# Kernel tuning notes

Measured on AMD Instinct MI355X. Metric: run time of the kernel, lower is better.

## Reference

```python
import jax, jax.numpy as jnp
import numpy as np

N, E, K = 20000, 320000, 4
IN, HID, OUT, HD = 512, 256, 128, 256


def setup_inputs() -> dict:
    key = jax.random.key(0)
    ks = jax.random.split(key, 12)
    def lin(k, fi, fo):
        return jax.random.normal(k, (fi, fo), jnp.float32) / np.sqrt(fi)
    return {
        "x": jax.random.normal(ks[0], (N, IN), jnp.float32),
        "edge_index": jax.random.randint(ks[1], (K, 2, E), 0, N),
        "value": jax.random.normal(ks[2], (K, 3), jnp.float32),
        "index": jax.random.randint(ks[3], (K, 2), 0, N),
        "W1": lin(ks[4], IN, HID),  "b1": jnp.zeros((HID,), jnp.float32),
        "W2": lin(ks[5], HID, OUT), "b2": jnp.zeros((OUT,), jnp.float32),
        "Wd": lin(ks[6], 2 * OUT + 3, HD), "bd": jnp.zeros((HD,), jnp.float32),
        "Wp": lin(ks[7], HD, 1),    "bp": jnp.zeros((1,), jnp.float32),
    }


def reference(x, edge_index, value, index, W1, b1, W2, b2, Wd, bd, Wp, bp):
    n = x.shape[0]
    loops = jnp.arange(n)

    def gcn(h, src, dst, W, b):
        # GCNConv: symmetric normalization with self-loops already in src/dst
        deg = jnp.zeros((n,), h.dtype).at[dst].add(1.0)
        dinv = jnp.where(deg > 0, deg ** -0.5, 0.0)
        norm = dinv[src] * dinv[dst]                      # [E+N]
        msg = (h @ W)[src] * norm[:, None]                # [E+N, F_out]
        return jnp.zeros((n, W.shape[1]), h.dtype).at[dst].add(msg) + b

    def encode(ei):
        src = jnp.concatenate([ei[0], loops])             # add self-loops
        dst = jnp.concatenate([ei[1], loops])
        h = jax.nn.relu(gcn(x, src, dst, W1, b1))
        return gcn(h, src, dst, W2, b2)                   # [N, OUT]

    def step(carry, inp):
        ei, val, idx = inp
        mu = encode(ei)
        h = jnp.concatenate([mu[idx[0]], mu[idx[1]], val])  # [2*OUT+3]
        o = jax.nn.relu(h @ Wd + bd)
        p = jax.nn.sigmoid(o @ Wp + bp)
        return carry, p[0]

    _, preds = jax.lax.scan(step, None, (edge_index, value, index))
    return preds  # [K]
```

## Files before the change

### kernel.cpp

```cpp
#include <hip/hip_runtime.h>
#include <hip/hip_bf16.h>


#define NN 20000
#define EE 320000
#define E4 (EE/4)
#define KK 4
#define FIN 512
#define FHID 256
#define FOUT 128
#define FHD 256
#define NH (2*FOUT+3)
#define CAP1 1024
#define MS2 128
#define BCAP 256
#define BMW 640

__device__ __forceinline__ float dinvf(int indeg) {
  return rsqrtf((float)(indeg + 1));
}

__global__ __launch_bounds__(256) void kz_zero(int4* __restrict__ p, int n4) {
  int i = blockIdx.x * 256 + threadIdx.x;
  if (i < n4) p[i] = make_int4(0, 0, 0, 0);
}

__global__ __launch_bounds__(256) void k12_scan_claim(const int* __restrict__ ei,
                                                      const int* __restrict__ idx,
                                                      int* __restrict__ cnt1,
                                                      int* __restrict__ L1src,
                                                      int* __restrict__ L1sel,
                                                      int* __restrict__ reg,
                                                      int* __restrict__ slotNode,
                                                      int* __restrict__ mslots,
                                                      unsigned* __restrict__ bA) {
  int k = blockIdx.y;
  int* rk = reg + (size_t)k * NN;
  unsigned* bAk = bA + k * BMW;
  int t0 = idx[2 * k], t1 = idx[2 * k + 1];
  if (blockIdx.x == 0 && threadIdx.x < 2) {
    int node = (threadIdx.x == 0) ? t0 : t1;
    if (atomicCAS(&rk[node], 0, -2) == 0) {
      int s = atomicAdd(&mslots[k], 1);
      if (s < MS2) {
        slotNode[k * MS2 + s] = node; rk[node] = s + 1;
        atomicOr(&bAk[node >> 5], 1u << (node & 31));
      }
    }
  }
  int e4 = blockIdx.x * blockDim.x + threadIdx.x;
  if (e4 >= E4) return;
  const int* srcp = ei + (size_t)k * 2 * EE;
  int4 d4 = ((const int4*)(srcp + EE))[e4];
  int ds[4] = {d4.x, d4.y, d4.z, d4.w};
  #pragma unroll
  for (int c = 0; c < 4; c++) {
    bool h0 = (ds[c] == t0), h1 = (ds[c] == t1);
    if (h0 || h1) {
      int u = srcp[e4 * 4 + c];
      if (h0) {
        int p = atomicAdd(&cnt1[k], 1);
        if (p < CAP1) { L1src[k * CAP1 + p] = u; L1sel[k * CAP1 + p] = 0; }
      }
      if (h1) {
        int p = atomicAdd(&cnt1[k], 1);
        if (p < CAP1) { L1src[k * CAP1 + p] = u; L1sel[k * CAP1 + p] = 1; }
      }
      if (atomicCAS(&rk[u], 0, -2) == 0) {
        int s = atomicAdd(&mslots[k], 1);
        if (s < MS2) {
          slotNode[k * MS2 + s] = u; rk[u] = s + 1;
          atomicOr(&bAk[u >> 5], 1u << (u & 31));
        }
      }
    }
  }
}

__global__ __launch_bounds__(256) void k3_scanL2(const int* __restrict__ ei,
                                                 const int* __restrict__ reg,
                                                 const unsigned* __restrict__ bA,
                                                 unsigned* __restrict__ bB,
                                                 int* __restrict__ bcnt,
                                                 int* __restrict__ bucket) {
  __shared__ unsigned lbA[BMW];
  int k = blockIdx.y;
  const unsigned* bAk = bA + k * BMW;
  for (int i = threadIdx.x; i < BMW; i += 256) lbA[i] = bAk[i];
  __syncthreads();
  int e4 = blockIdx.x * blockDim.x + threadIdx.x;
  if (e4 >= E4) return;
  const int* srcp = ei + (size_t)k * 2 * EE;
  int4 d4 = ((const int4*)(srcp + EE))[e4];
  const int* rk = reg + (size_t)k * NN;
  unsigned* bBk = bB + k * BMW;
  int ds[4] = {d4.x, d4.y, d4.z, d4.w};
  #pragma unroll
  for (int c = 0; c < 4; c++) {
    int d = ds[c];
    if ((lbA[d >> 5] >> (d & 31)) & 1u) {
      int s = rk[d] - 1;
      int u = srcp[e4 * 4 + c];
      int p = atomicAdd(&bcnt[k * MS2 + s], 1);
      if (p < BCAP) bucket[((size_t)k * MS2 + s) * BCAP + p] = u;
      atomicOr(&bBk[u >> 5], 1u << (u & 31));
    }
  }
}

__global__ __launch_bounds__(256) void k4_deg(const int* __restrict__ ei,
                                              const unsigned* __restrict__ bB,
                                              int* __restrict__ deg) {
  __shared__ unsigned lbB[BMW];
  int k = blockIdx.y;
  const unsigned* bBk = bB + k * BMW;
  for (int i = threadIdx.x; i < BMW; i += 256) lbB[i] = bBk[i];
  __syncthreads();
  int e4 = blockIdx.x * blockDim.x + threadIdx.x;
  if (e4 >= E4) return;
  const int4* dst4 = (const int4*)(ei + (size_t)k * 2 * EE + EE);
  int4 d4 = dst4[e4];
  int ds[4] = {d4.x, d4.y, d4.z, d4.w};
  #pragma unroll
  for (int c = 0; c < 4; c++) {
    int d = ds[c];
    if ((lbB[d >> 5] >> (d & 31)) & 1u) atomicAdd(&deg[k * NN + d], 1);
  }
}

__global__ __launch_bounds__(1024) void k5_slotmlp(const int* __restrict__ slotNode,
                                                   const int* __restrict__ mslots,
                                                   const int* __restrict__ bcnt,
                                                   const int* __restrict__ bucket,
                                                   const int* __restrict__ deg,
                                                   const float* __restrict__ x,
                                                   const float* __restrict__ W1,
                                                   const float* __restrict__ b1,
                                                   const float* __restrict__ W2,
                                                   float* __restrict__ HW2) {
  __shared__ float aggS[FIN];
  __shared__ float gtmp[FIN];
  __shared__ float part[4][FHID];
  __shared__ float hrow[FHID];
  __shared__ float part2[8][FOUT];
  __shared__ int   uS[BCAP];
  __shared__ float duS[BCAP];
  int k = blockIdx.y, s = blockIdx.x;
  if (s >= mslots[k]) return;
  int tid = threadIdx.x;
  int node = slotNode[k * MS2 + s];
  int rawbc = bcnt[k * MS2 + s];
  int nb = min(rawbc, BCAP);
  const int* bk = bucket + ((size_t)k * MS2 + s) * BCAP;
  for (int e = tid; e < nb; e += 1024) {
    int u = bk[e];
    uS[e] = u;
    duS[e] = dinvf(deg[k * NN + u]);
  }
  __syncthreads();
  float dn = dinvf(rawbc);
  int f = tid & (FIN - 1), half = tid >> 9;
  float a = (half == 0) ? dn * x[(size_t)node * FIN + f] : 0.f;
  for (int e = half; e < nb; e += 2) a += duS[e] * x[(size_t)uS[e] * FIN + f];
  if (half == 1) gtmp[f] = a;
  __syncthreads();
  if (half == 0) aggS[f] = dn * (a + gtmp[f]);
  __syncthreads();
  {
    int q = tid >> 8, j = tid & (FHID - 1);
    float acc = 0.f;
    const float* w1p = W1 + (size_t)(q * 128) * FHID + j;
    const float* ap = aggS + q * 128;
    #pragma unroll 8
    for (int kk = 0; kk < 128; kk++) acc += ap[kk] * w1p[(size_t)kk * FHID];
    part[q][j] = acc;
  }
  __syncthreads();
  if (tid < FHID) {
    float v = part[0][tid] + part[1][tid] + part[2][tid] + part[3][tid] + b1[tid];
    hrow[tid] = v > 0.f ? v : 0.f;
  }
  __syncthreads();
  {
    int p = tid >> 7, j = tid & (FOUT - 1);
    float a2 = 0.f;
    const float* w2p = W2 + (size_t)(p * 32) * FOUT + j;
    const float* hp = hrow + p * 32;
    #pragma unroll 8
    for (int kk = 0; kk < 32; kk++) a2 += hp[kk] * w2p[(size_t)kk * FOUT];
    part2[p][j] = a2;
  }
  __syncthreads();
  if (tid < FOUT) {
    float sv = part2[0][tid] + part2[1][tid] + part2[2][tid] + part2[3][tid] +
               part2[4][tid] + part2[5][tid] + part2[6][tid] + part2[7][tid];
    HW2[((size_t)k * MS2 + s) * FOUT + tid] = sv;
  }
}

__global__ __launch_bounds__(256) void k6_decode(const float* __restrict__ HW2,
                                                 const float* __restrict__ b2,
                                                 const int* __restrict__ cnt1,
                                                 const int* __restrict__ L1src,
                                                 const int* __restrict__ L1sel,
                                                 const int* __restrict__ idx,
                                                 const int* __restrict__ reg,
                                                 const int* __restrict__ bcnt,
                                                 const float* __restrict__ value,
                                                 const float* __restrict__ Wd,
                                                 const float* __restrict__ bd,
                                                 const float* __restrict__ Wp,
                                                 const float* __restrict__ bp,
                                                 float* __restrict__ out) {
  __shared__ float h[NH + 1];
  __shared__ float o[FHD];
  __shared__ float red[4];
  int k = blockIdx.x;
  int tid = threadIdx.x;
  const int* rk = reg + (size_t)k * NN;
  int n1 = min(cnt1[k], CAP1);
  int tsel = tid >> 7, j = tid & 127;
  int t = idx[2 * k + tsel];
  int tslot = rk[t] - 1;
  float dit = dinvf(bcnt[k * MS2 + tslot]);
  float acc = b2[j] + dit * dit * HW2[((size_t)k * MS2 + tslot) * FOUT + j];
  for (int i = 0; i < n1; i++) {
    if (L1sel[k * CAP1 + i] == tsel) {
      int s = L1src[k * CAP1 + i];
      int sslot = rk[s] - 1;
      float dis = dinvf(bcnt[k * MS2 + sslot]);
      acc += dis * dit * HW2[((size_t)k * MS2 + sslot) * FOUT + j];
    }
  }
  h[tsel * FOUT + j] = acc;
  if (tid < 3) h[2 * FOUT + tid] = value[k * 3 + tid];
  __syncthreads();
  float a2 = bd[tid];
  for (int i = 0; i < NH; i++) a2 += h[i] * Wd[(size_t)i * FHD + tid];
  o[tid] = a2 > 0.f ? a2 : 0.f;
  __syncthreads();
  float r = o[tid] * Wp[tid];
  for (int off2 = 32; off2 > 0; off2 >>= 1) r += __shfl_down(r, off2);
  if ((tid & 63) == 0) red[tid >> 6] = r;
  __syncthreads();
  if (tid == 0) {
    float ssum = red[0] + red[1] + red[2] + red[3] + bp[0];
    out[k] = 1.f / (1.f + expf(-ssum));
  }
}

extern "C" void kernel_launch(void* const* d_in, const int* in_sizes, int n_in,
                              void* d_out, int out_size, void* d_ws, size_t ws_size,
                              hipStream_t stream) {
  const float* x     = (const float*)d_in[0];
  const int*   ei    = (const int*)d_in[1];
  const float* value = (const float*)d_in[2];
  const int*   idx   = (const int*)d_in[3];
  const float* W1    = (const float*)d_in[4];
  const float* b1    = (const float*)d_in[5];
  const float* W2    = (const float*)d_in[6];
  const float* b2    = (const float*)d_in[7];
  const float* Wd    = (const float*)d_in[8];
  const float* bd    = (const float*)d_in[9];
  const float* Wp    = (const float*)d_in[10];
  const float* bp    = (const float*)d_in[11];
  float* out = (float*)d_out;

  char* ws = (char*)d_ws;
  size_t off = 0;
  auto alloc = [&](size_t bytes) -> void* {
    void* p = ws + off;
    off = (off + bytes + 255) & ~(size_t)255;
    return p;
  };
  size_t zints = (size_t)(2 * KK * NN + 2 * KK * BMW + KK * MS2 + 2 * KK);
  int* reg   = (int*)alloc(zints * sizeof(int));
  int* deg   = reg + KK * NN;
  unsigned* bA = (unsigned*)(deg + KK * NN);
  unsigned* bB = bA + KK * BMW;
  int* bcnt  = (int*)(bB + KK * BMW);
  int* cnt1  = bcnt + KK * MS2;
  int* mslots = cnt1 + KK;
  size_t zbytes = zints * sizeof(int);
  int* L1src = (int*)alloc((size_t)KK * CAP1 * sizeof(int));
  int* L1sel = (int*)alloc((size_t)KK * CAP1 * sizeof(int));
  int* slotNode = (int*)alloc((size_t)KK * MS2 * sizeof(int));
  int* bucket = (int*)alloc((size_t)KK * MS2 * BCAP * sizeof(int));
  float* HW2 = (float*)alloc((size_t)KK * MS2 * FOUT * sizeof(float));
  (void)ws_size; (void)in_sizes; (void)n_in; (void)out_size;

  int n4 = (int)((zbytes + 15) / 16);
  dim3 escan((E4 + 255) / 256, KK);

  kz_zero<<<(n4 + 255) / 256, 256, 0, stream>>>((int4*)reg, n4);
  k12_scan_claim<<<escan, 256, 0, stream>>>(ei, idx, cnt1, L1src, L1sel,
                                            reg, slotNode, mslots, bA);
  k3_scanL2<<<escan, 256, 0, stream>>>(ei, reg, bA, bB, bcnt, bucket);
  k4_deg<<<escan, 256, 0, stream>>>(ei, bB, deg);
  k5_slotmlp<<<dim3(MS2, KK), 1024, 0, stream>>>(slotNode, mslots, bcnt, bucket, deg,
                                                 x, W1, b1, W2, HW2);
  k6_decode<<<dim3(KK), 256, 0, stream>>>(HW2, b2, cnt1, L1src, L1sel, idx, reg, bcnt,
                                          value, Wd, bd, Wp, bp, out);
}
```

Before: 61.57 us.

## Split per-slot MLP into feature-quarter GEMV blocks and widen decode reduction

The fused per-slot 1024-thread MLP kernel is split in two. The first kernel uses four 256-thread blocks per slot, each aggregating one 128-feature quarter of x and multiplying it by the matching rows of W1 into a partial buffer. The second kernel sums those partials, applies bias and ReLU, and does the W2 GEMV. The decode kernel grows to 1024 threads and splits the Wd dot product four ways over input rows. This trades an extra launch and a global round trip of partial sums for more, smaller blocks spread across CUs and shorter serial loops.

```diff
diff --git a/kernel.cpp b/kernel.cpp
--- a/kernel.cpp
+++ b/kernel.cpp
@@ -128,120 +128,132 @@
   }
 }
 
-__global__ __launch_bounds__(1024) void k5_slotmlp(const int* __restrict__ slotNode,
-                                                   const int* __restrict__ mslots,
-                                                   const int* __restrict__ bcnt,
-                                                   const int* __restrict__ bucket,
-                                                   const int* __restrict__ deg,
-                                                   const float* __restrict__ x,
-                                                   const float* __restrict__ W1,
-                                                   const float* __restrict__ b1,
-                                                   const float* __restrict__ W2,
-                                                   float* __restrict__ HW2) {
-  __shared__ float aggS[FIN];
-  __shared__ float gtmp[FIN];
-  __shared__ float part[4][FHID];
-  __shared__ float hrow[FHID];
-  __shared__ float part2[8][FOUT];
+__global__ __launch_bounds__(256) void k5a_gemv1(const int* __restrict__ slotNode,
+                                                 const int* __restrict__ mslots,
+                                                 const int* __restrict__ bcnt,
+                                                 const int* __restrict__ bucket,
+                                                 const int* __restrict__ deg,
+                                                 const float* __restrict__ x,
+                                                 const float* __restrict__ W1,
+                                                 float* __restrict__ partQ) {
   __shared__ int   uS[BCAP];
   __shared__ float duS[BCAP];
-  int k = blockIdx.y, s = blockIdx.x;
+  __shared__ float aggq[128];
+  __shared__ float gtmp[128];
+  int k = blockIdx.y;
+  int s = blockIdx.x >> 2, q = blockIdx.x & 3;
   if (s >= mslots[k]) return;
   int tid = threadIdx.x;
   int node = slotNode[k * MS2 + s];
   int rawbc = bcnt[k * MS2 + s];
   int nb = min(rawbc, BCAP);
   const int* bk = bucket + ((size_t)k * MS2 + s) * BCAP;
-  for (int e = tid; e < nb; e += 1024) {
-    int u = bk[e];
-    uS[e] = u;
-    duS[e] = dinvf(deg[k * NN + u]);
+  if (tid < nb) {
+    int u = bk[tid];
+    uS[tid] = u;
+    duS[tid] = dinvf(deg[k * NN + u]);
   }
   __syncthreads();
   float dn = dinvf(rawbc);
-  int f = tid & (FIN - 1), half = tid >> 9;
-  float a = (half == 0) ? dn * x[(size_t)node * FIN + f] : 0.f;
-  for (int e = half; e < nb; e += 2) a += duS[e] * x[(size_t)uS[e] * FIN + f];
-  if (half == 1) gtmp[f] = a;
-  __syncthreads();
-  if (half == 0) aggS[f] = dn * (a + gtmp[f]);
-  __syncthreads();
+  int f = tid & 127, g = tid >> 7;
+  const float* xq = x + q * 128 + f;
+  float a = (g == 0) ? dn * xq[(size_t)node * FIN] : 0.f;
+  for (int e = g; e < nb; e += 2) a += duS[e] * xq[(size_t)uS[e] * FIN];
+  if (g == 1) gtmp[f] = a;
+  __syncthreads();
+  if (g == 0) aggq[f] = dn * (a + gtmp[f]);
+  __syncthreads();
+  float acc = 0.f;
+  const float* w1p = W1 + (size_t)(q * 128) * FHID + tid;
+  #pragma unroll 8
+  for (int kk = 0; kk < 128; kk++) acc += aggq[kk] * w1p[(size_t)kk * FHID];
+  partQ[(((size_t)k * MS2 + s) * 4 + q) * FHID + tid] = acc;
+}
+
+__global__ __launch_bounds__(256) void k5b_gemv2(const int* __restrict__ mslots,
+                                                 const float* __restrict__ partQ,
+                                                 const float* __restrict__ b1,
+                                                 const float* __restrict__ W2,
+                                                 float* __restrict__ HW2) {
+  __shared__ float hrow[FHID];
+  __shared__ float pr[FHID];
+  int k = blockIdx.y, s = blockIdx.x;
+  if (s >= mslots[k]) return;
+  int tid = threadIdx.x;
+  const float* pq = partQ + (((size_t)k * MS2 + s) * 4) * FHID;
   {
-    int q = tid >> 8, j = tid & (FHID - 1);
-    float acc = 0.f;
-    const float* w1p = W1 + (size_t)(q * 128) * FHID + j;
-    const float* ap = aggS + q * 128;
-    #pragma unroll 8
-    for (int kk = 0; kk < 128; kk++) acc += ap[kk] * w1p[(size_t)kk * FHID];
-    part[q][j] = acc;
-  }
-  __syncthreads();
-  if (tid < FHID) {
-    float v = part[0][tid] + part[1][tid] + part[2][tid] + part[3][tid] + b1[tid];
+    float v = pq[tid] + pq[FHID + tid] + pq[2 * FHID + tid] + pq[3 * FHID + tid] + b1[tid];
     hrow[tid] = v > 0.f ? v : 0.f;
   }
   __syncthreads();
-  {
-    int p = tid >> 7, j = tid & (FOUT - 1);
-    float a2 = 0.f;
-    const float* w2p = W2 + (size_t)(p * 32) * FOUT + j;
-    const float* hp = hrow + p * 32;
-    #pragma unroll 8
-    for (int kk = 0; kk < 32; kk++) a2 += hp[kk] * w2p[(size_t)kk * FOUT];
-    part2[p][j] = a2;
-  }
-  __syncthreads();
-  if (tid < FOUT) {
-    float sv = part2[0][tid] + part2[1][tid] + part2[2][tid] + part2[3][tid] +
-               part2[4][tid] + part2[5][tid] + part2[6][tid] + part2[7][tid];
-    HW2[((size_t)k * MS2 + s) * FOUT + tid] = sv;
-  }
-}
-
-__global__ __launch_bounds__(256) void k6_decode(const float* __restrict__ HW2,
-                                                 const float* __restrict__ b2,
-                                                 const int* __restrict__ cnt1,
-                                                 const int* __restrict__ L1src,
-                                                 const int* __restrict__ L1sel,
-                                                 const int* __restrict__ idx,
-                                                 const int* __restrict__ reg,
-                                                 const int* __restrict__ bcnt,
-                                                 const float* __restrict__ value,
-                                                 const float* __restrict__ Wd,
-                                                 const float* __restrict__ bd,
-                                                 const float* __restrict__ Wp,
-                                                 const float* __restrict__ bp,
-                                                 float* __restrict__ out) {
-  __shared__ float h[NH + 1];
-  __shared__ float o[FHD];
+  int half = tid >> 7, j = tid & 127;
+  float a = 0.f;
+  const float* w2p = W2 + (size_t)(half * 128) * FOUT + j;
+  #pragma unroll 8
+  for (int kk = 0; kk < 128; kk++) a += hrow[half * 128 + kk] * w2p[(size_t)kk * FOUT];
+  pr[tid] = a;
+  __syncthreads();
+  if (half == 0) HW2[((size_t)k * MS2 + s) * FOUT + j] = pr[j] + pr[128 + j];
+}
+
+__global__ __launch_bounds__(1024) void k6_decode(const float* __restrict__ HW2,
+                                                  const float* __restrict__ b2,
+                                                  const int* __restrict__ cnt1,
+                                                  const int* __restrict__ L1src,
+                                                  const int* __restrict__ L1sel,
+                                                  const int* __restrict__ idx,
+                                                  const int* __restrict__ reg,
+                                                  const int* __restrict__ bcnt,
+                                                  const float* __restrict__ value,
+                                                  const float* __restrict__ Wd,
+                                                  const float* __restrict__ bd,
+                                                  const float* __restrict__ Wp,
+                                                  const float* __restrict__ bp,
+                                                  float* __restrict__ out) {
+  __shared__ float hD[NH + 1];
+  __shared__ float oD[FHD];
+  __shared__ float pd[4][FHD];
   __shared__ float red[4];
   int k = blockIdx.x;
   int tid = threadIdx.x;
   const int* rk = reg + (size_t)k * NN;
   int n1 = min(cnt1[k], CAP1);
-  int tsel = tid >> 7, j = tid & 127;
-  int t = idx[2 * k + tsel];
-  int tslot = rk[t] - 1;
-  float dit = dinvf(bcnt[k * MS2 + tslot]);
-  float acc = b2[j] + dit * dit * HW2[((size_t)k * MS2 + tslot) * FOUT + j];
-  for (int i = 0; i < n1; i++) {
-    if (L1sel[k * CAP1 + i] == tsel) {
-      int s = L1src[k * CAP1 + i];
-      int sslot = rk[s] - 1;
-      float dis = dinvf(bcnt[k * MS2 + sslot]);
-      acc += dis * dit * HW2[((size_t)k * MS2 + sslot) * FOUT + j];
+  if (tid < 256) {
+    int tsel = tid >> 7, j = tid & 127;
+    int t = idx[2 * k + tsel];
+    int tslot = rk[t] - 1;
+    float dit = dinvf(bcnt[k * MS2 + tslot]);
+    float acc = b2[j] + dit * dit * HW2[((size_t)k * MS2 + tslot) * FOUT + j];
+    for (int i = 0; i < n1; i++) {
+      if (L1sel[k * CAP1 + i] == tsel) {
+        int sn = L1src[k * CAP1 + i];
+        int ss = rk[sn] - 1;
+        float dis = dinvf(bcnt[k * MS2 + ss]);
+        acc += dis * dit * HW2[((size_t)k * MS2 + ss) * FOUT + j];
+      }
     }
-  }
-  h[tsel * FOUT + j] = acc;
-  if (tid < 3) h[2 * FOUT + tid] = value[k * 3 + tid];
-  __syncthreads();
-  float a2 = bd[tid];
-  for (int i = 0; i < NH; i++) a2 += h[i] * Wd[(size_t)i * FHD + tid];
-  o[tid] = a2 > 0.f ? a2 : 0.f;
-  __syncthreads();
-  float r = o[tid] * Wp[tid];
-  for (int off2 = 32; off2 > 0; off2 >>= 1) r += __shfl_down(r, off2);
-  if ((tid & 63) == 0) red[tid >> 6] = r;
+    hD[tsel * FOUT + j] = acc;
+    if (tid < 3) hD[2 * FOUT + tid] = value[k * 3 + tid];
+  }
+  __syncthreads();
+  {
+    int jj = tid & 255, qd = tid >> 8;
+    int i0 = qd * 65, i1 = min(NH, i0 + 65);
+    float a2 = (qd == 0) ? bd[jj] : 0.f;
+    for (int i = i0; i < i1; i++) a2 += hD[i] * Wd[(size_t)i * FHD + jj];
+    pd[qd][jj] = a2;
+  }
+  __syncthreads();
+  if (tid < FHD) {
+    float v = pd[0][tid] + pd[1][tid] + pd[2][tid] + pd[3][tid];
+    oD[tid] = v > 0.f ? v : 0.f;
+  }
+  __syncthreads();
+  if (tid < FHD) {
+    float r = oD[tid] * Wp[tid];
+    for (int o2 = 32; o2 > 0; o2 >>= 1) r += __shfl_down(r, o2);
+    if ((tid & 63) == 0) red[tid >> 6] = r;
+  }
   __syncthreads();
   if (tid == 0) {
     float ssum = red[0] + red[1] + red[2] + red[3] + bp[0];
@@ -287,6 +299,7 @@
   int* slotNode = (int*)alloc((size_t)KK * MS2 * sizeof(int));
   int* bucket = (int*)alloc((size_t)KK * MS2 * BCAP * sizeof(int));
   float* HW2 = (float*)alloc((size_t)KK * MS2 * FOUT * sizeof(float));
+  float* partQ = (float*)alloc((size_t)KK * MS2 * 4 * FHID * sizeof(float));
   (void)ws_size; (void)in_sizes; (void)n_in; (void)out_size;
 
   int n4 = (int)((zbytes + 15) / 16);
@@ -297,8 +310,9 @@
                                             reg, slotNode, mslots, bA);
   k3_scanL2<<<escan, 256, 0, stream>>>(ei, reg, bA, bB, bcnt, bucket);
   k4_deg<<<escan, 256, 0, stream>>>(ei, bB, deg);
-  k5_slotmlp<<<dim3(MS2, KK), 1024, 0, stream>>>(slotNode, mslots, bcnt, bucket, deg,
-                                                 x, W1, b1, W2, HW2);
-  k6_decode<<<dim3(KK), 256, 0, stream>>>(HW2, b2, cnt1, L1src, L1sel, idx, reg, bcnt,
-                                          value, Wd, bd, Wp, bp, out);
-}
+  k5a_gemv1<<<dim3(MS2 * 4, KK), 256, 0, stream>>>(slotNode, mslots, bcnt, bucket,
+                                                   deg, x, W1, partQ);
+  k5b_gemv2<<<dim3(MS2, KK), 256, 0, stream>>>(mslots, partQ, b1, W2, HW2);
+  k6_decode<<<dim3(KK), 1024, 0, stream>>>(HW2, b2, cnt1, L1src, L1sel, idx, reg,
+                                           bcnt, value, Wd, bd, Wp, bp, out);
+}
```

After: 60.57 us. About the same (-1.6%).
